# Performance work log

Hardware: AMD Instinct MI355X
Metric: run time of the kernel (lower is better)

## Reference

```python
import jax, jax.numpy as jnp
import numpy as np

B, F, D, L, N = 2048, 40, 64, 3, 40  # batch, num_fields, embed_dim, num_layers, num_subspaces


def setup_inputs() -> dict:
    key = jax.random.key(0)
    inputs = jax.random.normal(key, (B, F, D), dtype=jnp.float32)
    # Parameters per layer, matching torch init exactly:
    #   W     = identity(D) repeated over out_subspaces -> [N, D, D]
    #   alpha = ones([num_fields, in_subspaces, out_subspaces]); in_subspaces == F for
    #           layer 0 and == N afterwards; with N == F all layers share shape [F, N, N]
    #   h     = ones([N, D, 1])
    W = jnp.broadcast_to(jnp.eye(D, dtype=jnp.float32), (L, N, D, D)).copy()
    alpha = jnp.ones((L, F, N, N), dtype=jnp.float32)
    h = jnp.ones((L, N, D, 1), dtype=jnp.float32)
    return {"inputs": inputs, "W": W, "alpha": alpha, "h": h}


def _fusion_layer(B0, Bi, W, alpha, h):
    # Original math: fusion[b,n,D,d] = sum_{f,i} alpha[f,i,n] * B0[b,f,D] * Bi[b,i,d]
    #                out[b,n,D]     = sum_d fusion[b,n,D,d] * W[n,D,d] * h[n,d]
    # Reordered to avoid the [b,f,n,D,d] outer-product tensor:
    M = W * h[:, :, 0][:, None, :]                 # [n, D, d] = W * h broadcast over D
    C = jnp.einsum('bid,nDd->binD', Bi, M)         # contract embed dim d first
    out = jnp.einsum('bfD,fin,binD->bnD', B0, alpha, C)
    return out


def reference(inputs, W, alpha, h):
    B_i = inputs
    for l in range(L):
        B_i = _fusion_layer(inputs, B_i, W[l], alpha[l], h[l])
    return B_i
```

## Files before the change

### kernel.cpp

```cpp
#include <hip/hip_runtime.h>


typedef __bf16 bf16x8 __attribute__((ext_vector_type(8)));
typedef float  f32x16 __attribute__((ext_vector_type(16)));

constexpr int BATCH = 2048;
constexpr int FDIM  = 40;
constexpr int DDIM  = 64;
constexpr int LAY   = 3;
constexpr int IPAD  = 64;
constexpr int FPAD  = 48;
constexpr int MB_BYTES  = DDIM * DDIM * 2;
constexpr int AT_BYTES  = IPAD * FPAD * 2;
constexpr int BUF_BYTES = MB_BYTES + AT_BYTES;

__device__ __forceinline__ unsigned short f2bf(float f) {
  union { float f; unsigned u; } v; v.f = f;
  unsigned r = v.u + 0x7fff + ((v.u >> 16) & 1);
  return (unsigned short)(r >> 16);
}

__device__ __forceinline__ void async16(const void* g, void* l) {
  __builtin_amdgcn_global_load_lds(
      (const __attribute__((address_space(1))) unsigned int*)g,
      (__attribute__((address_space(3))) unsigned int*)l, 16, 0, 0);
}

__global__ void prep_k(const float* __restrict__ W, const float* __restrict__ h,
                       const float* __restrict__ alpha, const float* __restrict__ inputs,
                       unsigned short* __restrict__ M, unsigned short* __restrict__ AT,
                       unsigned short* __restrict__ B0b, unsigned short* __restrict__ B0T) {
  int i = blockIdx.x * blockDim.x + threadIdx.x;
  const int nM  = LAY * FDIM * DDIM * DDIM;
  const int nAT = LAY * FDIM * IPAD * FPAD;
  const int nB  = BATCH * FDIM * DDIM;
  const int nT  = BATCH * DDIM * FPAD;
  if (i < nM) {
    int d  = i & 63;
    int ln = i >> 12;
    M[i] = f2bf(W[i] * h[ln * DDIM + d]);
    return;
  }
  i -= nM;
  if (i < nAT) {
    int f  = i % FPAD;
    int ii = (i / FPAD) % IPAD;
    int n  = (i / (FPAD * IPAD)) % FDIM;
    int l  = i / (FPAD * IPAD * FDIM);
    float v = 0.f;
    if (f < FDIM && ii < FDIM)
      v = alpha[(((size_t)l * FDIM + f) * FDIM + ii) * FDIM + n];
    AT[i] = f2bf(v);
    return;
  }
  i -= nAT;
  if (i < nB) { B0b[i] = f2bf(inputs[i]); return; }
  i -= nB;
  if (i >= nT) return;
  int b   = i / (DDIM * FPAD);
  int rem = i - b * (DDIM * FPAD);
  int d   = rem / FPAD;
  int f   = rem - d * FPAD;
  B0T[i] = (f < FDIM) ? f2bf(inputs[((size_t)b * FDIM + f) * DDIM + d]) : (unsigned short)0;
}

template <bool FINAL>
__global__ __launch_bounds__(256, 4) void layer_k(
    const unsigned short* __restrict__ Bi,
    const unsigned short* __restrict__ B0T,
    const unsigned short* __restrict__ Mt,
    const unsigned short* __restrict__ ATt,
    void* __restrict__ outp)
{
  __shared__ __align__(16) unsigned short smem[2 * BUF_BYTES / 2];

  const int tid  = threadIdx.x;
  const int lane = tid & 63;
  const int w    = tid >> 6;
  const int b2   = w >> 1;
  const int dt   = w & 1;
  const int c    = lane & 31;
  const int h    = lane >> 5;
  const int b    = blockIdx.x * 2 + b2;

  auto stage = [&](int n, int buf) {
    const unsigned short* Mn = Mt  + n * (DDIM * DDIM);
    const unsigned short* An = ATt + n * (IPAD * FPAD);
    char* base = (char*)smem + buf * BUF_BYTES;
#pragma unroll
    for (int r = 0; r < 2; ++r) {
      int p  = r * 256 + tid;
      int D  = p >> 3, pc = p & 7;
      int cd = pc ^ (D & 7);
      async16(Mn + D * DDIM + cd * 8, base + r * 4096 + w * 1024);
    }
    async16(An + tid * 8, base + MB_BYTES + w * 1024);
    if (w < 2)
      async16(An + (256 + tid) * 8, base + MB_BYTES + 4096 + w * 1024);
  };

  bf16x8 aBi[2][4];
#pragma unroll
  for (int it = 0; it < 2; ++it) {
    int row = it * 32 + c; if (row > FDIM - 1) row = FDIM - 1;
#pragma unroll
    for (int ks = 0; ks < 4; ++ks)
      aBi[it][ks] = *reinterpret_cast<const bf16x8*>(
          Bi + ((size_t)b * FDIM + row) * DDIM + ks * 16 + h * 8);
  }

  bf16x8 bT[3];
#pragma unroll
  for (int ks = 0; ks < 3; ++ks)
    bT[ks] = *reinterpret_cast<const bf16x8*>(
        B0T + ((size_t)b * DDIM + dt * 32 + c) * FPAD + ks * 16 + h * 8);

  stage(0, 0);

  for (int n = 0; n < FDIM; ++n) {
    __syncthreads();
    const int buf = n & 1;
    if (n + 1 < FDIM) stage(n + 1, buf ^ 1);

    const char* bufp = (const char*)smem + buf * BUF_BYTES;

    bf16x8 mb[4];
#pragma unroll
    for (int ks = 0; ks < 4; ++ks) {
      int D  = dt * 32 + c;
      int pc = (ks * 2 + h) ^ (D & 7);
      mb[ks] = *reinterpret_cast<const bf16x8*>(bufp + D * 128 + pc * 16);
    }

    float pout = 0.f;
#pragma unroll
    for (int it = 0; it < 2; ++it) {
      bf16x8 at[3];
#pragma unroll
      for (int ks = 0; ks < 3; ++ks)
        at[ks] = *reinterpret_cast<const bf16x8*>(
            bufp + MB_BYTES + ((it * 32 + c) * FPAD + ks * 16 + h * 8) * 2);

      f32x16 aC = {0,0,0,0,0,0,0,0,0,0,0,0,0,0,0,0};
      f32x16 aR = {0,0,0,0,0,0,0,0,0,0,0,0,0,0,0,0};
#pragma unroll
      for (int ks = 0; ks < 4; ++ks)
        aC = __builtin_amdgcn_mfma_f32_32x32x16_bf16(aBi[it][ks], mb[ks], aC, 0, 0, 0);
#pragma unroll
      for (int ks = 0; ks < 3; ++ks)
        aR = __builtin_amdgcn_mfma_f32_32x32x16_bf16(at[ks], bT[ks], aR, 0, 0, 0);

      float t0 = 0.f, t1 = 0.f, t2 = 0.f, t3 = 0.f;
#pragma unroll
      for (int r = 0; r < 4; ++r) {
        t0 += aC[r] * aR[r];         t1 += aC[r + 4] * aR[r + 4];
        t2 += aC[r + 8] * aR[r + 8]; t3 += aC[r + 12] * aR[r + 12];
      }
      pout += (t0 + t1) + (t2 + t3);
    }

    float v = pout + __shfl_xor(pout, 32, 64);
    if (lane < 32) {
      size_t off = ((size_t)b * FDIM + n) * DDIM + dt * 32 + lane;
      if (FINAL) ((float*)outp)[off] = v;
      else       ((unsigned short*)outp)[off] = f2bf(v);
    }
  }
}

extern "C" void kernel_launch(void* const* d_in, const int* in_sizes, int n_in,
                              void* d_out, int out_size, void* d_ws, size_t ws_size,
                              hipStream_t stream) {
  const float* inputs = (const float*)d_in[0];
  const float* W      = (const float*)d_in[1];
  const float* alpha  = (const float*)d_in[2];
  const float* h      = (const float*)d_in[3];

  char* ws = (char*)d_ws;
  const size_t S   = (size_t)BATCH * FDIM * DDIM * 2;
  const size_t ST  = (size_t)BATCH * DDIM * FPAD * 2;
  unsigned short* Bi1 = (unsigned short*)(ws);
  unsigned short* Bi2 = (unsigned short*)(ws + S);
  unsigned short* B0b = (unsigned short*)(ws + 2 * S);
  unsigned short* B0T = (unsigned short*)(ws + 3 * S);
  unsigned short* Mb  = (unsigned short*)(ws + 3 * S + ST);
  unsigned short* ATb = (unsigned short*)(ws + 3 * S + ST + (size_t)LAY * FDIM * DDIM * DDIM * 2);

  const int nPrep = LAY * FDIM * DDIM * DDIM + LAY * FDIM * IPAD * FPAD
                  + BATCH * FDIM * DDIM + BATCH * DDIM * FPAD;
  prep_k<<<(nPrep + 255) / 256, 256, 0, stream>>>(W, h, alpha, inputs, Mb, ATb, B0b, B0T);

  dim3 grid(BATCH / 2), blk(256);
  const size_t mL = (size_t)FDIM * DDIM * DDIM;
  const size_t aL = (size_t)FDIM * IPAD * FPAD;
  layer_k<false><<<grid, blk, 0, stream>>>(B0b, B0T, Mb, ATb, Bi1);
  layer_k<false><<<grid, blk, 0, stream>>>(Bi1, B0T, Mb + mL, ATb + aL, Bi2);
  layer_k<true ><<<grid, blk, 0, stream>>>(Bi2, B0T, Mb + 2 * mL, ATb + 2 * aL, d_out);
}
```

Measured before the change: 292.7 us.

## Split layer kernel over output-subspace groups and loop batch per block

Each block of the layer kernel now handles two output subspaces and loops over a slice of 16 batch elements, instead of handling two batch elements and streaming all 40 subspaces through double-buffered LDS. The per-subspace M and alpha tiles are loaded once per block and reused across the batch elements, which removes the per-iteration barrier and staging. In exchange, each batch's Bi and B0T operands are re-read from global memory by 20 different blocks, raising L2 traffic. The prep kernel is also vectorised to handle four elements per thread.

```diff
diff --git a/kernel.cpp b/kernel.cpp
--- a/kernel.cpp
+++ b/kernel.cpp
@@ -3,6 +3,7 @@
 
 typedef __bf16 bf16x8 __attribute__((ext_vector_type(8)));
 typedef float  f32x16 __attribute__((ext_vector_type(16)));
+typedef unsigned short us4 __attribute__((ext_vector_type(4)));
 
 constexpr int BATCH = 2048;
 constexpr int FDIM  = 40;
@@ -10,6 +11,10 @@
 constexpr int LAY   = 3;
 constexpr int IPAD  = 64;
 constexpr int FPAD  = 48;
+constexpr int NSPAN = 2;
+constexpr int NG    = FDIM / NSPAN;
+constexpr int BG    = 128;
+constexpr int BPB   = BATCH / BG;
 constexpr int MB_BYTES  = DDIM * DDIM * 2;
 constexpr int AT_BYTES  = IPAD * FPAD * 2;
 constexpr int BUF_BYTES = MB_BYTES + AT_BYTES;
@@ -30,38 +35,60 @@
                        const float* __restrict__ alpha, const float* __restrict__ inputs,
                        unsigned short* __restrict__ M, unsigned short* __restrict__ AT,
                        unsigned short* __restrict__ B0b, unsigned short* __restrict__ B0T) {
-  int i = blockIdx.x * blockDim.x + threadIdx.x;
-  const int nM  = LAY * FDIM * DDIM * DDIM;
-  const int nAT = LAY * FDIM * IPAD * FPAD;
-  const int nB  = BATCH * FDIM * DDIM;
-  const int nT  = BATCH * DDIM * FPAD;
-  if (i < nM) {
-    int d  = i & 63;
-    int ln = i >> 12;
-    M[i] = f2bf(W[i] * h[ln * DDIM + d]);
+  int j = blockIdx.x * blockDim.x + threadIdx.x;
+  const int nM4 = LAY * FDIM * DDIM * DDIM / 4;
+  const int nA4 = LAY * FDIM * IPAD * FPAD / 4;
+  const int nB4 = BATCH * FDIM * DDIM / 4;
+  const int nT4 = BATCH * DDIM * FPAD / 4;
+  if (j < nM4) {
+    int e  = j * 4;
+    int d  = e & 63;
+    int ln = e >> 12;
+    float4 wv = *reinterpret_cast<const float4*>(W + e);
+    float4 hv = *reinterpret_cast<const float4*>(h + ln * DDIM + d);
+    us4 o = { f2bf(wv.x * hv.x), f2bf(wv.y * hv.y), f2bf(wv.z * hv.z), f2bf(wv.w * hv.w) };
+    *reinterpret_cast<us4*>(M + e) = o;
     return;
   }
-  i -= nM;
-  if (i < nAT) {
-    int f  = i % FPAD;
-    int ii = (i / FPAD) % IPAD;
-    int n  = (i / (FPAD * IPAD)) % FDIM;
-    int l  = i / (FPAD * IPAD * FDIM);
-    float v = 0.f;
-    if (f < FDIM && ii < FDIM)
-      v = alpha[(((size_t)l * FDIM + f) * FDIM + ii) * FDIM + n];
-    AT[i] = f2bf(v);
+  j -= nM4;
+  if (j < nA4) {
+    int e  = j * 4;
+    int f  = e % FPAD;
+    int ii = (e / FPAD) % IPAD;
+    int n  = (e / (FPAD * IPAD)) % FDIM;
+    int l  = e / (FPAD * IPAD * FDIM);
+    us4 o = {0, 0, 0, 0};
+    if (ii < FDIM) {
+#pragma unroll
+      for (int k = 0; k < 4; ++k)
+        if (f + k < FDIM)
+          o[k] = f2bf(alpha[(((size_t)l * FDIM + f + k) * FDIM + ii) * FDIM + n]);
+    }
+    *reinterpret_cast<us4*>(AT + e) = o;
     return;
   }
-  i -= nAT;
-  if (i < nB) { B0b[i] = f2bf(inputs[i]); return; }
-  i -= nB;
-  if (i >= nT) return;
-  int b   = i / (DDIM * FPAD);
-  int rem = i - b * (DDIM * FPAD);
-  int d   = rem / FPAD;
-  int f   = rem - d * FPAD;
-  B0T[i] = (f < FDIM) ? f2bf(inputs[((size_t)b * FDIM + f) * DDIM + d]) : (unsigned short)0;
+  j -= nA4;
+  if (j < nB4) {
+    int e = j * 4;
+    float4 v = *reinterpret_cast<const float4*>(inputs + e);
+    us4 o = { f2bf(v.x), f2bf(v.y), f2bf(v.z), f2bf(v.w) };
+    *reinterpret_cast<us4*>(B0b + e) = o;
+    return;
+  }
+  j -= nB4;
+  if (j >= nT4) return;
+  {
+    int e  = j * 4;
+    int f  = e % FPAD;
+    int d  = (e / FPAD) % DDIM;
+    int b  = e / (FPAD * DDIM);
+    us4 o = {0, 0, 0, 0};
+#pragma unroll
+    for (int k = 0; k < 4; ++k)
+      if (f + k < FDIM)
+        o[k] = f2bf(inputs[((size_t)b * FDIM + f + k) * DDIM + d]);
+    *reinterpret_cast<us4*>(B0T + e) = o;
+  }
 }
 
 template <bool FINAL>
@@ -72,7 +99,7 @@
     const unsigned short* __restrict__ ATt,
     void* __restrict__ outp)
 {
-  __shared__ __align__(16) unsigned short smem[2 * BUF_BYTES / 2];
+  __shared__ __align__(16) unsigned short smem[NSPAN * BUF_BYTES / 2];
 
   const int tid  = threadIdx.x;
   const int lane = tid & 63;
@@ -81,12 +108,16 @@
   const int dt   = w & 1;
   const int c    = lane & 31;
   const int h    = lane >> 5;
-  const int b    = blockIdx.x * 2 + b2;
-
-  auto stage = [&](int n, int buf) {
-    const unsigned short* Mn = Mt  + n * (DDIM * DDIM);
-    const unsigned short* An = ATt + n * (IPAD * FPAD);
-    char* base = (char*)smem + buf * BUF_BYTES;
+  const int ng   = blockIdx.x / BG;
+  const int bg   = blockIdx.x % BG;
+  const int n0   = ng * NSPAN;
+  const int bBase = bg * BPB;
+
+#pragma unroll
+  for (int nn = 0; nn < NSPAN; ++nn) {
+    const unsigned short* Mn = Mt  + (n0 + nn) * (DDIM * DDIM);
+    const unsigned short* An = ATt + (n0 + nn) * (IPAD * FPAD);
+    char* base = (char*)smem + nn * BUF_BYTES;
 #pragma unroll
     for (int r = 0; r < 2; ++r) {
       int p  = r * 256 + tid;
@@ -97,73 +128,72 @@
     async16(An + tid * 8, base + MB_BYTES + w * 1024);
     if (w < 2)
       async16(An + (256 + tid) * 8, base + MB_BYTES + 4096 + w * 1024);
-  };
-
-  bf16x8 aBi[2][4];
-#pragma unroll
-  for (int it = 0; it < 2; ++it) {
-    int row = it * 32 + c; if (row > FDIM - 1) row = FDIM - 1;
-#pragma unroll
-    for (int ks = 0; ks < 4; ++ks)
-      aBi[it][ks] = *reinterpret_cast<const bf16x8*>(
-          Bi + ((size_t)b * FDIM + row) * DDIM + ks * 16 + h * 8);
-  }
-
-  bf16x8 bT[3];
-#pragma unroll
-  for (int ks = 0; ks < 3; ++ks)
-    bT[ks] = *reinterpret_cast<const bf16x8*>(
-        B0T + ((size_t)b * DDIM + dt * 32 + c) * FPAD + ks * 16 + h * 8);
-
-  stage(0, 0);
-
-  for (int n = 0; n < FDIM; ++n) {
-    __syncthreads();
-    const int buf = n & 1;
-    if (n + 1 < FDIM) stage(n + 1, buf ^ 1);
-
-    const char* bufp = (const char*)smem + buf * BUF_BYTES;
-
-    bf16x8 mb[4];
-#pragma unroll
-    for (int ks = 0; ks < 4; ++ks) {
-      int D  = dt * 32 + c;
-      int pc = (ks * 2 + h) ^ (D & 7);
-      mb[ks] = *reinterpret_cast<const bf16x8*>(bufp + D * 128 + pc * 16);
-    }
-
-    float pout = 0.f;
+  }
+  __syncthreads();
+
+  for (int bi = 0; bi < BPB / 2; ++bi) {
+    const int b = bBase + bi * 2 + b2;
+
+    bf16x8 aBi[2][4];
 #pragma unroll
     for (int it = 0; it < 2; ++it) {
-      bf16x8 at[3];
-#pragma unroll
-      for (int ks = 0; ks < 3; ++ks)
-        at[ks] = *reinterpret_cast<const bf16x8*>(
-            bufp + MB_BYTES + ((it * 32 + c) * FPAD + ks * 16 + h * 8) * 2);
-
-      f32x16 aC = {0,0,0,0,0,0,0,0,0,0,0,0,0,0,0,0};
-      f32x16 aR = {0,0,0,0,0,0,0,0,0,0,0,0,0,0,0,0};
+      int row = it * 32 + c; if (row > FDIM - 1) row = FDIM - 1;
 #pragma unroll
       for (int ks = 0; ks < 4; ++ks)
-        aC = __builtin_amdgcn_mfma_f32_32x32x16_bf16(aBi[it][ks], mb[ks], aC, 0, 0, 0);
-#pragma unroll
-      for (int ks = 0; ks < 3; ++ks)
-        aR = __builtin_amdgcn_mfma_f32_32x32x16_bf16(at[ks], bT[ks], aR, 0, 0, 0);
-
-      float t0 = 0.f, t1 = 0.f, t2 = 0.f, t3 = 0.f;
-#pragma unroll
-      for (int r = 0; r < 4; ++r) {
-        t0 += aC[r] * aR[r];         t1 += aC[r + 4] * aR[r + 4];
-        t2 += aC[r + 8] * aR[r + 8]; t3 += aC[r + 12] * aR[r + 12];
+        aBi[it][ks] = *reinterpret_cast<const bf16x8*>(
+            Bi + ((size_t)b * FDIM + row) * DDIM + ks * 16 + h * 8);
+    }
+    bf16x8 bT[3];
+#pragma unroll
+    for (int ks = 0; ks < 3; ++ks)
+      bT[ks] = *reinterpret_cast<const bf16x8*>(
+          B0T + ((size_t)b * DDIM + dt * 32 + c) * FPAD + ks * 16 + h * 8);
+
+#pragma unroll
+    for (int nn = 0; nn < NSPAN; ++nn) {
+      const char* bufp = (const char*)smem + nn * BUF_BYTES;
+
+      bf16x8 mb[4];
+#pragma unroll
+      for (int ks = 0; ks < 4; ++ks) {
+        int D  = dt * 32 + c;
+        int pc = (ks * 2 + h) ^ (D & 7);
+        mb[ks] = *reinterpret_cast<const bf16x8*>(bufp + D * 128 + pc * 16);
       }
-      pout += (t0 + t1) + (t2 + t3);
-    }
-
-    float v = pout + __shfl_xor(pout, 32, 64);
-    if (lane < 32) {
-      size_t off = ((size_t)b * FDIM + n) * DDIM + dt * 32 + lane;
-      if (FINAL) ((float*)outp)[off] = v;
-      else       ((unsigned short*)outp)[off] = f2bf(v);
+
+      float pout = 0.f;
+#pragma unroll
+      for (int it = 0; it < 2; ++it) {
+        bf16x8 at[3];
+#pragma unroll
+        for (int ks = 0; ks < 3; ++ks)
+          at[ks] = *reinterpret_cast<const bf16x8*>(
+              bufp + MB_BYTES + ((it * 32 + c) * FPAD + ks * 16 + h * 8) * 2);
+
+        f32x16 aC = {0,0,0,0,0,0,0,0,0,0,0,0,0,0,0,0};
+        f32x16 aR = {0,0,0,0,0,0,0,0,0,0,0,0,0,0,0,0};
+#pragma unroll
+        for (int ks = 0; ks < 4; ++ks)
+          aC = __builtin_amdgcn_mfma_f32_32x32x16_bf16(aBi[it][ks], mb[ks], aC, 0, 0, 0);
+#pragma unroll
+        for (int ks = 0; ks < 3; ++ks)
+          aR = __builtin_amdgcn_mfma_f32_32x32x16_bf16(at[ks], bT[ks], aR, 0, 0, 0);
+
+        float t0 = 0.f, t1 = 0.f, t2 = 0.f, t3 = 0.f;
+#pragma unroll
+        for (int r = 0; r < 4; ++r) {
+          t0 += aC[r] * aR[r];         t1 += aC[r + 4] * aR[r + 4];
+          t2 += aC[r + 8] * aR[r + 8]; t3 += aC[r + 12] * aR[r + 12];
+        }
+        pout += (t0 + t1) + (t2 + t3);
+      }
+
+      float v = pout + __shfl_xor(pout, 32, 64);
+      if (lane < 32) {
+        size_t off = ((size_t)b * FDIM + (n0 + nn)) * DDIM + dt * 32 + lane;
+        if (FINAL) ((float*)outp)[off] = v;
+        else       ((unsigned short*)outp)[off] = f2bf(v);
+      }
     }
   }
 }
@@ -186,11 +216,11 @@
   unsigned short* Mb  = (unsigned short*)(ws + 3 * S + ST);
   unsigned short* ATb = (unsigned short*)(ws + 3 * S + ST + (size_t)LAY * FDIM * DDIM * DDIM * 2);
 
-  const int nPrep = LAY * FDIM * DDIM * DDIM + LAY * FDIM * IPAD * FPAD
-                  + BATCH * FDIM * DDIM + BATCH * DDIM * FPAD;
-  prep_k<<<(nPrep + 255) / 256, 256, 0, stream>>>(W, h, alpha, inputs, Mb, ATb, B0b, B0T);
-
-  dim3 grid(BATCH / 2), blk(256);
+  const int nPrep4 = (LAY * FDIM * DDIM * DDIM + LAY * FDIM * IPAD * FPAD
+                    + BATCH * FDIM * DDIM + BATCH * DDIM * FPAD) / 4;
+  prep_k<<<(nPrep4 + 255) / 256, 256, 0, stream>>>(W, h, alpha, inputs, Mb, ATb, B0b, B0T);
+
+  dim3 grid(NG * BG), blk(256);
   const size_t mL = (size_t)FDIM * DDIM * DDIM;
   const size_t aL = (size_t)FDIM * IPAD * FPAD;
   layer_k<false><<<grid, blk, 0, stream>>>(B0b, B0T, Mb, ATb, Bi1);
```

Result: slower. 594.7 us (+103.2%).
